# Optimization experiments

Measured on AMD Instinct MI355X. Metric: run time of the kernel, lower is better.

The kernel has to match this reference:

```python
import jax, jax.numpy as jnp
import numpy as np

N_NODES = 100000
N_EDGES = 640000
D_FEAT = 128
HIDDEN = 128
FINAL = 64
N_GRAPHS = 128


def setup_inputs() -> dict:
    key = jax.random.key(0)
    ks = jax.random.split(key, 8)
    x = jax.random.normal(ks[0], (N_NODES, D_FEAT), dtype=jnp.float32)
    edge_index = jax.random.randint(ks[1], (2, N_EDGES), 0, N_NODES, dtype=jnp.int64)
    batch = jnp.sort(jax.random.randint(ks[2], (N_NODES,), 0, N_GRAPHS, dtype=jnp.int64))
    # SAGEConv params: lin_l (aggregated neighbors, with bias), lin_r (self, no bias)
    W_l = jax.random.normal(ks[3], (HIDDEN, D_FEAT), dtype=jnp.float32) / np.sqrt(D_FEAT)
    b_l = jnp.zeros((HIDDEN,), dtype=jnp.float32)
    W_r = jax.random.normal(ks[4], (HIDDEN, D_FEAT), dtype=jnp.float32) / np.sqrt(D_FEAT)
    # Final linear head on column_stack([max_pool, mean_pool])
    W_lin = jax.random.normal(ks[5], (FINAL, 2 * HIDDEN), dtype=jnp.float32) / np.sqrt(2 * HIDDEN)
    b_lin = jnp.zeros((FINAL,), dtype=jnp.float32)
    return {"x": x, "edge_index": edge_index, "batch": batch,
            "W_l": W_l, "b_l": b_l, "W_r": W_r, "W_lin": W_lin, "b_lin": b_lin}


def reference(x, edge_index, batch, W_l, b_l, W_r, W_lin, b_lin):
    N = x.shape[0]
    src, dst = edge_index[0], edge_index[1]
    # SAGEConv: mean-aggregate neighbor messages src -> dst
    agg = jax.ops.segment_sum(x[src], dst, num_segments=N)  # [N, D]
    deg = jax.ops.segment_sum(jnp.ones_like(src, dtype=x.dtype), dst, num_segments=N)
    agg = agg / jnp.maximum(deg, 1.0)[:, None]
    h = agg @ W_l.T + b_l + x @ W_r.T  # [N, HIDDEN]
    h = jax.nn.relu(h)
    # global max / mean pool over graphs in batch
    x_max = jax.ops.segment_max(h, batch, num_segments=N_GRAPHS)  # [G, HIDDEN]
    cnt = jax.ops.segment_sum(jnp.ones((N,), h.dtype), batch, num_segments=N_GRAPHS)
    x_mean = jax.ops.segment_sum(h, batch, num_segments=N_GRAPHS) / jnp.maximum(cnt, 1.0)[:, None]
    z = jnp.concatenate([x_max, x_mean], axis=1)  # [G, 2*HIDDEN]
    # dropout is identity in eval mode (training=False)
    return z @ W_lin.T + b_lin
```

## Files before the change

### kernel.cpp

```cpp
#include <hip/hip_runtime.h>
#include <math.h>

#define NN 100000
#define NE 640000
#define NG 128
#define NF 64
#define MAXDEG 32

typedef __attribute__((ext_vector_type(8))) short short8;
typedef __attribute__((ext_vector_type(4))) float floatx4;

__device__ __forceinline__ unsigned short bf16_rne(float v) {
    unsigned u = __float_as_uint(v);
    return (unsigned short)((u + 0x7FFF + ((u >> 16) & 1)) >> 16);
}
__device__ __forceinline__ void split2(float f0, float f1, unsigned& H, unsigned& L) {
    unsigned short h0 = bf16_rne(f0), h1 = bf16_rne(f1);
    float r0 = f0 - __uint_as_float((unsigned)h0 << 16);
    float r1 = f1 - __uint_as_float((unsigned)h1 << 16);
    H = (unsigned)h0 | ((unsigned)h1 << 16);
    L = (unsigned)bf16_rne(r0) | ((unsigned)bf16_rne(r1) << 16);
}

__global__ __launch_bounds__(256) void k_zero(int* __restrict__ cnt,
                                              float* __restrict__ pools) {
    int idx = blockIdx.x * 256 + threadIdx.x;
    if (idx < NN) cnt[idx] = 0;
    else if (idx < NN + 2 * NG * 128) pools[idx - NN] = 0.f;
}

__global__ __launch_bounds__(256) void k_prep(const int* __restrict__ ei,
                                              int* __restrict__ cnt,
                                              int* __restrict__ slot,
                                              const float* __restrict__ Wl,
                                              const float* __restrict__ Wr,
                                              unsigned short* __restrict__ Bhi,
                                              unsigned short* __restrict__ Blo) {
    if (blockIdx.x < 128) {
        int idx = blockIdx.x * 256 + threadIdx.x;
        int k = idx >> 7;
        int j = idx & 127;
        float v = (k < 128) ? Wl[j * 128 + k] : Wr[j * 128 + (k - 128)];
        int c = k >> 5, nb = j >> 4;
        int l = (j & 15) + (((k >> 3) & 3) << 4);
        int e = k & 7;
        int off = ((c * 8 + nb) * 64 + l) * 8 + e;
        unsigned short hb = bf16_rne(v);
        float hf = __uint_as_float((unsigned)hb << 16);
        Bhi[off] = hb;
        Blo[off] = bf16_rne(v - hf);
    } else {
        int e = (blockIdx.x - 128) * 256 + threadIdx.x;
        if (e >= NE) return;
        int src = ei[e];
        int dst = ei[NE + e];
        int pos = atomicAdd(&cnt[dst], 1);
        if (pos < MAXDEG) slot[dst * MAXDEG + pos] = src;
    }
}

__global__ __launch_bounds__(256, 6) void k_fused(const float* __restrict__ x,
                                                  const int* __restrict__ slot,
                                                  const int* __restrict__ cnt,
                                                  const int* __restrict__ batch,
                                                  const unsigned short* __restrict__ Bhi,
                                                  const unsigned short* __restrict__ Blo,
                                                  const float* __restrict__ bl,
                                                  float* __restrict__ pmax,
                                                  float* __restrict__ psum) {
    __shared__ unsigned short Ahi_s[2 * 4 * 64 * 8];
    __shared__ unsigned short Alo_s[2 * 4 * 64 * 8];
    __shared__ int sbatch[32];
    int tid = threadIdx.x;
    int wave = tid >> 6, lane = tid & 63;
    int g = lane >> 4, i = lane & 15;
    int gb48 = lane & 48;
    int n0 = blockIdx.x * 32;
    if (tid < 32) sbatch[tid] = batch[n0 + tid];

    const float4* x4 = (const float4*)x;
    int wm = wave >> 1, wn = wave & 1;
    floatx4 acc[4];
    #pragma unroll
    for (int n = 0; n < 4; ++n) acc[n] = (floatx4){0.f, 0.f, 0.f, 0.f};

    float4 self0[2], self1[2];

    #pragma unroll
    for (int p = 0; p < 2; ++p) {
        int ln = wave * 8 + p * 4 + g;
        int n = n0 + ln;
        int ctrue = cnt[n];
        float inv = 1.f / fmaxf((float)ctrue, 1.f);
        int c = ctrue > MAXDEG ? MAXDEG : ctrue;
        int idx0 = slot[n * MAXDEG + i];
        int idx1 = slot[n * MAXDEG + 16 + i];
        int cmax = c;
        cmax = max(cmax, __shfl_xor(cmax, 16));
        cmax = max(cmax, __shfl_xor(cmax, 32));
        float4 a0 = make_float4(0.f, 0.f, 0.f, 0.f);
        float4 a1 = make_float4(0.f, 0.f, 0.f, 0.f);
        size_t selfb = (size_t)n * 32 + 2 * i;
        int c1 = cmax < 16 ? cmax : 16;
        for (int e = 0; e < c1; e += 4) {
            float4 v0[4], v1[4];
            bool ok[4];
            #pragma unroll
            for (int u = 0; u < 4; ++u) {
                int ee = e + u;
                int sv = __shfl(idx0, gb48 + (ee & 15));
                ok[u] = ee < c;
                size_t b = ok[u] ? ((size_t)sv * 32 + 2 * i) : selfb;
                v0[u] = x4[b];
                v1[u] = x4[b + 1];
            }
            #pragma unroll
            for (int u = 0; u < 4; ++u) {
                if (ok[u]) {
                    a0.x += v0[u].x; a0.y += v0[u].y; a0.z += v0[u].z; a0.w += v0[u].w;
                    a1.x += v1[u].x; a1.y += v1[u].y; a1.z += v1[u].z; a1.w += v1[u].w;
                }
            }
        }
        if (cmax > 16) {
            for (int e = 16; e < cmax; e += 4) {
                float4 v0[4], v1[4];
                bool ok[4];
                #pragma unroll
                for (int u = 0; u < 4; ++u) {
                    int ee = e + u;
                    int sv = __shfl(idx1, gb48 + ((ee - 16) & 15));
                    ok[u] = ee < c;
                    size_t b = ok[u] ? ((size_t)sv * 32 + 2 * i) : selfb;
                    v0[u] = x4[b];
                    v1[u] = x4[b + 1];
                }
                #pragma unroll
                for (int u = 0; u < 4; ++u) {
                    if (ok[u]) {
                        a0.x += v0[u].x; a0.y += v0[u].y; a0.z += v0[u].z; a0.w += v0[u].w;
                        a1.x += v1[u].x; a1.y += v1[u].y; a1.z += v1[u].z; a1.w += v1[u].w;
                    }
                }
            }
        }
        a0.x *= inv; a0.y *= inv; a0.z *= inv; a0.w *= inv;
        a1.x *= inv; a1.y *= inv; a1.z *= inv; a1.w *= inv;
        int base = (((ln >> 4) * 4 + (i >> 2)) * 64 + (ln & 15) + ((i & 3) << 4)) * 8;
        uint4 H, L;
        split2(a0.x, a0.y, H.x, L.x);
        split2(a0.z, a0.w, H.y, L.y);
        split2(a1.x, a1.y, H.z, L.z);
        split2(a1.z, a1.w, H.w, L.w);
        *(uint4*)&Ahi_s[base] = H;
        *(uint4*)&Alo_s[base] = L;
        self0[p] = x4[selfb];
        self1[p] = x4[selfb + 1];
    }
    __syncthreads();
    #pragma unroll
    for (int c = 0; c < 4; ++c) {
        short8 ah = *(const short8*)&Ahi_s[((wm * 4 + c) * 64 + lane) * 8];
        short8 al = *(const short8*)&Alo_s[((wm * 4 + c) * 64 + lane) * 8];
        #pragma unroll
        for (int n = 0; n < 4; ++n) {
            int nb = wn * 4 + n;
            int off = ((c * 8 + nb) * 64 + lane) * 8;
            short8 bh = *(const short8*)&Bhi[off];
            short8 bo = *(const short8*)&Blo[off];
            acc[n] = __builtin_amdgcn_mfma_f32_16x16x32_bf16(ah, bh, acc[n], 0, 0, 0);
            acc[n] = __builtin_amdgcn_mfma_f32_16x16x32_bf16(ah, bo, acc[n], 0, 0, 0);
            acc[n] = __builtin_amdgcn_mfma_f32_16x16x32_bf16(al, bh, acc[n], 0, 0, 0);
        }
    }
    __syncthreads();

    #pragma unroll
    for (int p = 0; p < 2; ++p) {
        int ln = wave * 8 + p * 4 + g;
        int base = (((ln >> 4) * 4 + (i >> 2)) * 64 + (ln & 15) + ((i & 3) << 4)) * 8;
        uint4 H, L;
        split2(self0[p].x, self0[p].y, H.x, L.x);
        split2(self0[p].z, self0[p].w, H.y, L.y);
        split2(self1[p].x, self1[p].y, H.z, L.z);
        split2(self1[p].z, self1[p].w, H.w, L.w);
        *(uint4*)&Ahi_s[base] = H;
        *(uint4*)&Alo_s[base] = L;
    }
    __syncthreads();
    #pragma unroll
    for (int c = 0; c < 4; ++c) {
        short8 ah = *(const short8*)&Ahi_s[((wm * 4 + c) * 64 + lane) * 8];
        short8 al = *(const short8*)&Alo_s[((wm * 4 + c) * 64 + lane) * 8];
        #pragma unroll
        for (int n = 0; n < 4; ++n) {
            int nb = wn * 4 + n;
            int off = (((c + 4) * 8 + nb) * 64 + lane) * 8;
            short8 bh = *(const short8*)&Bhi[off];
            short8 bo = *(const short8*)&Blo[off];
            acc[n] = __builtin_amdgcn_mfma_f32_16x16x32_bf16(ah, bh, acc[n], 0, 0, 0);
            acc[n] = __builtin_amdgcn_mfma_f32_16x16x32_bf16(ah, bo, acc[n], 0, 0, 0);
            acc[n] = __builtin_amdgcn_mfma_f32_16x16x32_bf16(al, bh, acc[n], 0, 0, 0);
        }
    }

    int colb = wn * 64 + i;
    float v[4][4];
    #pragma unroll
    for (int n = 0; n < 4; ++n) {
        float bv = bl[colb + n * 16];
        #pragma unroll
        for (int r = 0; r < 4; ++r) v[n][r] = fmaxf(acc[n][r] + bv, 0.f);
    }
    int myg[4];
    #pragma unroll
    for (int r = 0; r < 4; ++r) myg[r] = sbatch[wm * 16 + g * 4 + r];
    int gfirst = sbatch[wm * 16];
    int glast  = sbatch[wm * 16 + 15];
    for (int gg = gfirst; gg <= glast; ++gg) {
        #pragma unroll
        for (int n = 0; n < 4; ++n) {
            float mx = 0.f, sm = 0.f;
            #pragma unroll
            for (int r = 0; r < 4; ++r) {
                if (myg[r] == gg) { mx = fmaxf(mx, v[n][r]); sm += v[n][r]; }
            }
            mx = fmaxf(mx, __shfl_xor(mx, 16));
            mx = fmaxf(mx, __shfl_xor(mx, 32));
            sm += __shfl_xor(sm, 16);
            sm += __shfl_xor(sm, 32);
            if (lane < 16) {
                atomicMax((unsigned*)&pmax[gg * 128 + colb + n * 16], __float_as_uint(mx));
                atomicAdd(&psum[gg * 128 + colb + n * 16], sm);
            }
        }
    }
}

__global__ __launch_bounds__(128) void k_pool2head(const float* __restrict__ pmax,
                                                   const float* __restrict__ psum,
                                                   const int* __restrict__ batch,
                                                   const float* __restrict__ Wlin,
                                                   const float* __restrict__ blin,
                                                   float* __restrict__ out) {
    int g = blockIdx.x;
    int t = threadIdx.x;
    int lo = 0, hi = NN;
    while (lo < hi) { int mid = (lo + hi) >> 1; if (batch[mid] < g) lo = mid + 1; else hi = mid; }
    int start = lo;
    hi = NN;
    while (lo < hi) { int mid = (lo + hi) >> 1; if (batch[mid] < g + 1) lo = mid + 1; else hi = mid; }
    int cntg = lo - start;
    __shared__ float z[256];
    z[t]       = pmax[g * 128 + t];
    z[128 + t] = psum[g * 128 + t] / fmaxf((float)cntg, 1.f);
    __syncthreads();
    if (t < 64) {
        float acc = blin[t];
        const float* w = &Wlin[t * 256];
        #pragma unroll 8
        for (int c = 0; c < 256; ++c) acc = fmaf(z[c], w[c], acc);
        out[g * 64 + t] = acc;
    }
}

extern "C" void kernel_launch(void* const* d_in, const int* in_sizes, int n_in,
                              void* d_out, int out_size, void* d_ws, size_t ws_size,
                              hipStream_t stream) {
    const float* x     = (const float*)d_in[0];
    const int*   ei    = (const int*)d_in[1];
    const int*   batch = (const int*)d_in[2];
    const float* Wl    = (const float*)d_in[3];
    const float* bl    = (const float*)d_in[4];
    const float* Wr    = (const float*)d_in[5];
    const float* Wlin  = (const float*)d_in[6];
    const float* blin  = (const float*)d_in[7];
    float* out = (float*)d_out;

    char* ws = (char*)d_ws;
    int*   cnt  = (int*)(ws);
    int*   slot = (int*)(ws + 409600);
    float* pmax = (float*)(ws + 13209600);
    float* psum = (float*)(ws + 13275136);
    unsigned short* Bhi = (unsigned short*)(ws + 13340672);
    unsigned short* Blo = (unsigned short*)(ws + 13406208);

    k_zero<<<(NN + 2 * NG * 128 + 255) / 256, 256, 0, stream>>>(cnt, pmax);
    k_prep<<<128 + (NE + 255) / 256, 256, 0, stream>>>(ei, cnt, slot, Wl, Wr, Bhi, Blo);
    k_fused<<<NN / 32, 256, 0, stream>>>(x, slot, cnt, batch, Bhi, Blo, bl, pmax, psum);
    k_pool2head<<<NG, 128, 0, stream>>>(pmax, psum, batch, Wlin, blin, out);
}
```

Before: 213.2 us.

## Gather neighbor features from a bf16 copy of x to halve gather traffic

Adds a prep stage that converts x to a bf16 copy in workspace, and the neighbor-mean gather now reads 16-byte bf16 rows instead of 32-byte fp32 rows, widening each value to fp32 before accumulating. The self features are reloaded in fp32 after the first MFMA phase instead of being held in registers, and the occupancy hint rises from 6 to 8 waves per SIMD. This targets the random-gather memory traffic and register pressure. In exchange it adds a full extra pass over x (read fp32, write bf16) and lowers the precision of the aggregated neighbor values.

```diff
diff --git a/kernel.cpp b/kernel.cpp
--- a/kernel.cpp
+++ b/kernel.cpp
@@ -21,6 +21,8 @@
     H = (unsigned)h0 | ((unsigned)h1 << 16);
     L = (unsigned)bf16_rne(r0) | ((unsigned)bf16_rne(r1) << 16);
 }
+__device__ __forceinline__ float blo(unsigned w) { return __uint_as_float(w << 16); }
+__device__ __forceinline__ float bhi(unsigned w) { return __uint_as_float(w & 0xFFFF0000u); }
 
 __global__ __launch_bounds__(256) void k_zero(int* __restrict__ cnt,
                                               float* __restrict__ pools) {
@@ -32,6 +34,8 @@
 __global__ __launch_bounds__(256) void k_prep(const int* __restrict__ ei,
                                               int* __restrict__ cnt,
                                               int* __restrict__ slot,
+                                              const float* __restrict__ x,
+                                              unsigned short* __restrict__ xb,
                                               const float* __restrict__ Wl,
                                               const float* __restrict__ Wr,
                                               unsigned short* __restrict__ Bhi,
@@ -49,17 +53,29 @@
         float hf = __uint_as_float((unsigned)hb << 16);
         Bhi[off] = hb;
         Blo[off] = bf16_rne(v - hf);
-    } else {
+    } else if (blockIdx.x < 128 + 2500) {
         int e = (blockIdx.x - 128) * 256 + threadIdx.x;
         if (e >= NE) return;
         int src = ei[e];
         int dst = ei[NE + e];
         int pos = atomicAdd(&cnt[dst], 1);
         if (pos < MAXDEG) slot[dst * MAXDEG + pos] = src;
-    }
-}
-
-__global__ __launch_bounds__(256, 6) void k_fused(const float* __restrict__ x,
+    } else {
+        int t = (blockIdx.x - 2628) * 256 + threadIdx.x;
+        const float4* xf = (const float4*)x;
+        float4 f0 = xf[(size_t)t * 2];
+        float4 f1 = xf[(size_t)t * 2 + 1];
+        uint4 o;
+        o.x = (unsigned)bf16_rne(f0.x) | ((unsigned)bf16_rne(f0.y) << 16);
+        o.y = (unsigned)bf16_rne(f0.z) | ((unsigned)bf16_rne(f0.w) << 16);
+        o.z = (unsigned)bf16_rne(f1.x) | ((unsigned)bf16_rne(f1.y) << 16);
+        o.w = (unsigned)bf16_rne(f1.z) | ((unsigned)bf16_rne(f1.w) << 16);
+        ((uint4*)xb)[t] = o;
+    }
+}
+
+__global__ __launch_bounds__(256, 8) void k_fused(const float* __restrict__ x,
+                                                  const unsigned short* __restrict__ xb,
                                                   const int* __restrict__ slot,
                                                   const int* __restrict__ cnt,
                                                   const int* __restrict__ batch,
@@ -78,13 +94,12 @@
     int n0 = blockIdx.x * 32;
     if (tid < 32) sbatch[tid] = batch[n0 + tid];
 
+    const uint4* xb4 = (const uint4*)xb;
     const float4* x4 = (const float4*)x;
     int wm = wave >> 1, wn = wave & 1;
     floatx4 acc[4];
     #pragma unroll
     for (int n = 0; n < 4; ++n) acc[n] = (floatx4){0.f, 0.f, 0.f, 0.f};
-
-    float4 self0[2], self1[2];
 
     #pragma unroll
     for (int p = 0; p < 2; ++p) {
@@ -98,64 +113,61 @@
         int cmax = c;
         cmax = max(cmax, __shfl_xor(cmax, 16));
         cmax = max(cmax, __shfl_xor(cmax, 32));
-        float4 a0 = make_float4(0.f, 0.f, 0.f, 0.f);
-        float4 a1 = make_float4(0.f, 0.f, 0.f, 0.f);
-        size_t selfb = (size_t)n * 32 + 2 * i;
+        size_t selfbb = (size_t)n * 16 + i;
+        float a[8] = {0.f, 0.f, 0.f, 0.f, 0.f, 0.f, 0.f, 0.f};
         int c1 = cmax < 16 ? cmax : 16;
         for (int e = 0; e < c1; e += 4) {
-            float4 v0[4], v1[4];
+            uint4 v[4];
             bool ok[4];
             #pragma unroll
             for (int u = 0; u < 4; ++u) {
                 int ee = e + u;
                 int sv = __shfl(idx0, gb48 + (ee & 15));
                 ok[u] = ee < c;
-                size_t b = ok[u] ? ((size_t)sv * 32 + 2 * i) : selfb;
-                v0[u] = x4[b];
-                v1[u] = x4[b + 1];
+                v[u] = xb4[ok[u] ? ((size_t)sv * 16 + i) : selfbb];
             }
             #pragma unroll
             for (int u = 0; u < 4; ++u) {
                 if (ok[u]) {
-                    a0.x += v0[u].x; a0.y += v0[u].y; a0.z += v0[u].z; a0.w += v0[u].w;
-                    a1.x += v1[u].x; a1.y += v1[u].y; a1.z += v1[u].z; a1.w += v1[u].w;
+                    a[0] += blo(v[u].x); a[1] += bhi(v[u].x);
+                    a[2] += blo(v[u].y); a[3] += bhi(v[u].y);
+                    a[4] += blo(v[u].z); a[5] += bhi(v[u].z);
+                    a[6] += blo(v[u].w); a[7] += bhi(v[u].w);
                 }
             }
         }
         if (cmax > 16) {
             for (int e = 16; e < cmax; e += 4) {
-                float4 v0[4], v1[4];
+                uint4 v[4];
                 bool ok[4];
                 #pragma unroll
                 for (int u = 0; u < 4; ++u) {
                     int ee = e + u;
                     int sv = __shfl(idx1, gb48 + ((ee - 16) & 15));
                     ok[u] = ee < c;
-                    size_t b = ok[u] ? ((size_t)sv * 32 + 2 * i) : selfb;
-                    v0[u] = x4[b];
-                    v1[u] = x4[b + 1];
+                    v[u] = xb4[ok[u] ? ((size_t)sv * 16 + i) : selfbb];
                 }
                 #pragma unroll
                 for (int u = 0; u < 4; ++u) {
                     if (ok[u]) {
-                        a0.x += v0[u].x; a0.y += v0[u].y; a0.z += v0[u].z; a0.w += v0[u].w;
-                        a1.x += v1[u].x; a1.y += v1[u].y; a1.z += v1[u].z; a1.w += v1[u].w;
+                        a[0] += blo(v[u].x); a[1] += bhi(v[u].x);
+                        a[2] += blo(v[u].y); a[3] += bhi(v[u].y);
+                        a[4] += blo(v[u].z); a[5] += bhi(v[u].z);
+                        a[6] += blo(v[u].w); a[7] += bhi(v[u].w);
                     }
                 }
             }
         }
-        a0.x *= inv; a0.y *= inv; a0.z *= inv; a0.w *= inv;
-        a1.x *= inv; a1.y *= inv; a1.z *= inv; a1.w *= inv;
+        #pragma unroll
+        for (int k = 0; k < 8; ++k) a[k] *= inv;
         int base = (((ln >> 4) * 4 + (i >> 2)) * 64 + (ln & 15) + ((i & 3) << 4)) * 8;
         uint4 H, L;
-        split2(a0.x, a0.y, H.x, L.x);
-        split2(a0.z, a0.w, H.y, L.y);
-        split2(a1.x, a1.y, H.z, L.z);
-        split2(a1.z, a1.w, H.w, L.w);
+        split2(a[0], a[1], H.x, L.x);
+        split2(a[2], a[3], H.y, L.y);
+        split2(a[4], a[5], H.z, L.z);
+        split2(a[6], a[7], H.w, L.w);
         *(uint4*)&Ahi_s[base] = H;
         *(uint4*)&Alo_s[base] = L;
-        self0[p] = x4[selfb];
-        self1[p] = x4[selfb + 1];
     }
     __syncthreads();
     #pragma unroll
@@ -178,12 +190,15 @@
     #pragma unroll
     for (int p = 0; p < 2; ++p) {
         int ln = wave * 8 + p * 4 + g;
+        int n = n0 + ln;
+        float4 s0 = x4[(size_t)n * 32 + 2 * i];
+        float4 s1 = x4[(size_t)n * 32 + 2 * i + 1];
         int base = (((ln >> 4) * 4 + (i >> 2)) * 64 + (ln & 15) + ((i & 3) << 4)) * 8;
         uint4 H, L;
-        split2(self0[p].x, self0[p].y, H.x, L.x);
-        split2(self0[p].z, self0[p].w, H.y, L.y);
-        split2(self1[p].x, self1[p].y, H.z, L.z);
-        split2(self1[p].z, self1[p].w, H.w, L.w);
+        split2(s0.x, s0.y, H.x, L.x);
+        split2(s0.z, s0.w, H.y, L.y);
+        split2(s1.x, s1.y, H.z, L.z);
+        split2(s1.z, s1.w, H.w, L.w);
         *(uint4*)&Ahi_s[base] = H;
         *(uint4*)&Alo_s[base] = L;
     }
@@ -278,15 +293,16 @@
     float* out = (float*)d_out;
 
     char* ws = (char*)d_ws;
-    int*   cnt  = (int*)(ws);
-    int*   slot = (int*)(ws + 409600);
-    float* pmax = (float*)(ws + 13209600);
-    float* psum = (float*)(ws + 13275136);
-    unsigned short* Bhi = (unsigned short*)(ws + 13340672);
-    unsigned short* Blo = (unsigned short*)(ws + 13406208);
+    int*            cnt  = (int*)(ws);
+    int*            slot = (int*)(ws + 409600);
+    unsigned short* xb   = (unsigned short*)(ws + 13209600);
+    float*          pmax = (float*)(ws + 38809600);
+    float*          psum = (float*)(ws + 38875136);
+    unsigned short* Bhi  = (unsigned short*)(ws + 38940672);
+    unsigned short* Blo  = (unsigned short*)(ws + 39006208);
 
     k_zero<<<(NN + 2 * NG * 128 + 255) / 256, 256, 0, stream>>>(cnt, pmax);
-    k_prep<<<128 + (NE + 255) / 256, 256, 0, stream>>>(ei, cnt, slot, Wl, Wr, Bhi, Blo);
-    k_fused<<<NN / 32, 256, 0, stream>>>(x, slot, cnt, batch, Bhi, Blo, bl, pmax, psum);
+    k_prep<<<128 + 2500 + 6250, 256, 0, stream>>>(ei, cnt, slot, x, xb, Wl, Wr, Bhi, Blo);
+    k_fused<<<NN / 32, 256, 0, stream>>>(x, xb, slot, cnt, batch, Bhi, Blo, bl, pmax, psum);
     k_pool2head<<<NG, 128, 0, stream>>>(pmax, psum, batch, Wlin, blin, out);
 }
```

After: 197.2 us. -7.5%, faster.
